# Kernel tuning notes

Measured on AMD Instinct MI355X. Metric: run time of the kernel, lower is better.

## Reference

```python
import jax, jax.numpy as jnp
import numpy as np

B, C, T = 2, 2, 4
N_SRC = 49152   # npix at level 6 (12 * 4^6)
N_TGT = 12288   # npix at level 5 (12 * 4^5)
D = 128


def setup_inputs() -> dict:
    key = jax.random.key(0)
    k1, k2, k3, k4 = jax.random.split(key, 4)
    x = jax.random.normal(k1, (B, C, T, N_SRC, D), dtype=jnp.float32)
    parent_map = jax.random.randint(k2, (N_SRC,), 0, N_TGT)
    W = jax.random.normal(k3, (D, D), dtype=jnp.float32) * 0.05  # Conv1d kernel_size=1 weight [out,in]
    b = jax.random.normal(k4, (D,), dtype=jnp.float32) * 0.05    # Conv1d bias
    return {"x": x, "parent_map": parent_map, "W": W, "b": b}


def reference(x, parent_map, W, b):
    # HEALPix downsample: scatter-add mean pooling over parent_map, then 1x1 conv.
    Bs, Cs, Ts, N, Dd = x.shape
    # flatten (b c t) and put pixel axis first for segment_sum: [N, BCT, D]
    x2 = x.reshape(Bs * Cs * Ts, N, Dd).transpose(1, 0, 2)
    sums = jax.ops.segment_sum(x2, parent_map, num_segments=N_TGT)          # [N_TGT, BCT, D]
    cnt = jax.ops.segment_sum(jnp.ones((N,), x.dtype), parent_map, num_segments=N_TGT)
    mean = sums / jnp.clip(cnt, 1e-6)[:, None, None]
    # 1x1 Conv1d over channel dim D: y = W @ mean + b
    out = jnp.einsum('mbd,ed->mbe', mean, W) + b                            # [N_TGT, BCT, D]
    return out.transpose(1, 0, 2).reshape(Bs, Cs, Ts, N_TGT, Dd)
```

## Files before the change

kernel.cpp:

```cpp
#include <hip/hip_runtime.h>
#include <stdint.h>

#define NSRC 49152
#define NTGT 12288
#define DIM  128
#define BCT  16
#define MPER 8
#define ROWS (MPER*BCT)
#define CAP  32

using short8  = __attribute__((ext_vector_type(8))) short;
using short4v = __attribute__((ext_vector_type(4))) short;
using bf16x8  = __attribute__((ext_vector_type(8))) __bf16;
using f32x4   = __attribute__((ext_vector_type(4))) float;

__device__ __forceinline__ short f2bf(float f){
  unsigned int u = __float_as_uint(f);
  return (short)((u + 0x7fffu + ((u >> 16) & 1u)) >> 16);
}

__global__ void k_scatter(const int* __restrict__ pm,
                          int* __restrict__ counts, int* __restrict__ child){
  int i = blockIdx.x * blockDim.x + threadIdx.x;
  if (i < NSRC){
    int p = pm[i];
    int pos = atomicAdd(&counts[p], 1);
    if (pos < CAP) child[p * CAP + pos] = i;
  }
}

__global__ void k_wprep(const float* __restrict__ W, short* __restrict__ Wt){
  int t  = blockIdx.x * blockDim.x + threadIdx.x;
  int e  = t & 127;
  int kk = t >> 7;
  const float4* src = (const float4*)(W + (size_t)e * DIM + kk * 8);
  float4 u = src[0], v = src[1];
  short8 h;
  h[0]=f2bf(u.x); h[1]=f2bf(u.y); h[2]=f2bf(u.z); h[3]=f2bf(u.w);
  h[4]=f2bf(v.x); h[5]=f2bf(v.y); h[6]=f2bf(v.z); h[7]=f2bf(v.w);
  *reinterpret_cast<short8*>(Wt + ((size_t)kk * 128 + e) * 8) = h;
}

__global__ __launch_bounds__(256, 4) void k_fused(
    const float* __restrict__ x, const short* __restrict__ Wt,
    const float* __restrict__ bias,
    const int* __restrict__ counts, const int* __restrict__ child,
    float* __restrict__ out)
{
  __shared__ __align__(16) short s_mean[ROWS * DIM];
  const int tid = threadIdx.x;
  const int m0  = blockIdx.x * MPER;

  {
    const int o = tid & 7;
    #pragma unroll
    for (int it = 0; it < 4; ++it){
      const int r   = it * 32 + (tid >> 3);
      const int m   = m0 + (r >> 4);
      const int bct = r & 15;
      int cnt = counts[m]; cnt = (cnt > CAP) ? CAP : cnt;
      const int* cl = child + (size_t)m * CAP;
      const float* rowb = x + (size_t)bct * NSRC * DIM;
      float4 acc[4];
      #pragma unroll
      for (int s = 0; s < 4; ++s) acc[s] = make_float4(0.f, 0.f, 0.f, 0.f);
      int c = 0;
      for (; c + 1 < cnt; c += 2){
        const int n0 = cl[c], n1 = cl[c + 1];
        const float4* p0 = (const float4*)(rowb + (size_t)n0 * DIM) + o;
        const float4* p1 = (const float4*)(rowb + (size_t)n1 * DIM) + o;
        float4 v0[4], v1[4];
        #pragma unroll
        for (int s = 0; s < 4; ++s) v0[s] = p0[s * 8];
        #pragma unroll
        for (int s = 0; s < 4; ++s) v1[s] = p1[s * 8];
        #pragma unroll
        for (int s = 0; s < 4; ++s){
          acc[s].x += v0[s].x + v1[s].x; acc[s].y += v0[s].y + v1[s].y;
          acc[s].z += v0[s].z + v1[s].z; acc[s].w += v0[s].w + v1[s].w;
        }
      }
      if (c < cnt){
        const int n0 = cl[c];
        const float4* p0 = (const float4*)(rowb + (size_t)n0 * DIM) + o;
        #pragma unroll
        for (int s = 0; s < 4; ++s){
          float4 v = p0[s * 8];
          acc[s].x += v.x; acc[s].y += v.y; acc[s].z += v.z; acc[s].w += v.w;
        }
      }
      const float inv = (cnt > 0) ? (1.0f / (float)cnt) : 0.0f;
      const int rsw = (r & 7) << 3;
      #pragma unroll
      for (int s = 0; s < 4; ++s){
        const int col = s * 32 + o * 4;
        short4v h;
        h[0] = f2bf(acc[s].x * inv); h[1] = f2bf(acc[s].y * inv);
        h[2] = f2bf(acc[s].z * inv); h[3] = f2bf(acc[s].w * inv);
        *reinterpret_cast<short4v*>(&s_mean[r * DIM + (col ^ rsw)]) = h;
      }
    }
  }

  __syncthreads();

  {
    const int w  = tid >> 6;
    const int l  = tid & 63;
    const int lr = l & 15;
    const int kg = l >> 4;
    f32x4 acc[2][8];
    #pragma unroll
    for (int i = 0; i < 2; ++i)
      #pragma unroll
      for (int n = 0; n < 8; ++n) acc[i][n] = (f32x4){0.f, 0.f, 0.f, 0.f};

    #pragma unroll 1
    for (int ks = 0; ks < 4; ++ks){
      const int k = ks * 32 + kg * 8;
      bf16x8 af[2];
      #pragma unroll
      for (int i = 0; i < 2; ++i){
        const int row = w * 32 + i * 16 + lr;
        af[i] = *reinterpret_cast<bf16x8*>(&s_mean[row * DIM + (k ^ ((row & 7) << 3))]);
      }
      const short* wp = Wt + ((size_t)(ks * 4 + kg) * 128 + lr) * 8;
      #pragma unroll
      for (int n = 0; n < 8; ++n){
        bf16x8 bfr = *reinterpret_cast<const bf16x8*>(wp + n * 128);
        acc[0][n] = __builtin_amdgcn_mfma_f32_16x16x32_bf16(af[0], bfr, acc[0][n], 0, 0, 0);
        acc[1][n] = __builtin_amdgcn_mfma_f32_16x16x32_bf16(af[1], bfr, acc[1][n], 0, 0, 0);
      }
    }

    float bv[8];
    #pragma unroll
    for (int n = 0; n < 8; ++n) bv[n] = bias[n * 16 + lr];

    #pragma unroll
    for (int i = 0; i < 2; ++i){
      #pragma unroll
      for (int j = 0; j < 4; ++j){
        const int gr  = w * 32 + i * 16 + (l >> 4) * 4 + j;
        const int m   = m0 + (gr >> 4);
        const int bct = gr & 15;
        float* po = out + ((size_t)bct * NTGT + m) * DIM;
        #pragma unroll
        for (int n = 0; n < 8; ++n) po[n * 16 + lr] = acc[i][n][j] + bv[n];
      }
    }
  }
}

extern "C" void kernel_launch(void* const* d_in, const int* in_sizes, int n_in,
                              void* d_out, int out_size, void* d_ws, size_t ws_size,
                              hipStream_t stream) {
  const float* x    = (const float*)d_in[0];
  const int*   pm   = (const int*)  d_in[1];
  const float* W    = (const float*)d_in[2];
  const float* bias = (const float*)d_in[3];
  float* out = (float*)d_out;

  int*   counts = (int*)d_ws;
  int*   child  = counts + NTGT;
  short* Wt     = (short*)(child + NTGT * CAP);

  hipMemsetAsync(counts, 0, NTGT * sizeof(int), stream);
  k_scatter<<<NSRC/256, 256, 0, stream>>>(pm, counts, child);
  k_wprep  <<<8, 256, 0, stream>>>(W, Wt);
  k_fused  <<<NTGT/MPER, 256, 0, stream>>>(x, Wt, bias, counts, child, out);
}
```

Baseline: 137.9 us.

## Stage output through LDS for coalesced nontemporal stores; merge setup kernels

The output epilogue now writes MFMA accumulators into a padded LDS tile in two rounds, then reads them back so each wavefront emits contiguous 16-byte nontemporal stores per bct row. This replaces the scattered 4-byte global stores of the old epilogue. Separately, the scatter and weight-prep kernels are merged into one launch to cut launch overhead. The change adds extra syncthreads and LDS traffic in the epilogue, and the LDS buffer grows from 32KB to about 33KB, which may affect occupancy.

```diff
diff --git a/kernel.cpp b/kernel.cpp
--- a/kernel.cpp
+++ b/kernel.cpp
@@ -4,10 +4,10 @@
 #define NSRC 49152
 #define NTGT 12288
 #define DIM  128
-#define BCT  16
 #define MPER 8
-#define ROWS (MPER*BCT)
+#define ROWS (MPER*16)
 #define CAP  32
+#define OSTR 132
 
 using short8  = __attribute__((ext_vector_type(8))) short;
 using short4v = __attribute__((ext_vector_type(4))) short;
@@ -19,26 +19,26 @@
   return (short)((u + 0x7fffu + ((u >> 16) & 1u)) >> 16);
 }
 
-__global__ void k_scatter(const int* __restrict__ pm,
-                          int* __restrict__ counts, int* __restrict__ child){
-  int i = blockIdx.x * blockDim.x + threadIdx.x;
-  if (i < NSRC){
+__global__ void k_setup(const int* __restrict__ pm,
+                        int* __restrict__ counts, int* __restrict__ child,
+                        const float* __restrict__ W, short* __restrict__ Wt){
+  const int b = blockIdx.x;
+  if (b < 192){
+    int i = b * 256 + threadIdx.x;
     int p = pm[i];
     int pos = atomicAdd(&counts[p], 1);
     if (pos < CAP) child[p * CAP + pos] = i;
+  } else {
+    int t  = (b - 192) * 256 + threadIdx.x;
+    int e  = t & 127;
+    int kk = t >> 7;
+    const float4* src = (const float4*)(W + (size_t)e * DIM + kk * 8);
+    float4 u = src[0], v = src[1];
+    short8 h;
+    h[0]=f2bf(u.x); h[1]=f2bf(u.y); h[2]=f2bf(u.z); h[3]=f2bf(u.w);
+    h[4]=f2bf(v.x); h[5]=f2bf(v.y); h[6]=f2bf(v.z); h[7]=f2bf(v.w);
+    *reinterpret_cast<short8*>(Wt + ((size_t)kk * 128 + e) * 8) = h;
   }
-}
-
-__global__ void k_wprep(const float* __restrict__ W, short* __restrict__ Wt){
-  int t  = blockIdx.x * blockDim.x + threadIdx.x;
-  int e  = t & 127;
-  int kk = t >> 7;
-  const float4* src = (const float4*)(W + (size_t)e * DIM + kk * 8);
-  float4 u = src[0], v = src[1];
-  short8 h;
-  h[0]=f2bf(u.x); h[1]=f2bf(u.y); h[2]=f2bf(u.z); h[3]=f2bf(u.w);
-  h[4]=f2bf(v.x); h[5]=f2bf(v.y); h[6]=f2bf(v.z); h[7]=f2bf(v.w);
-  *reinterpret_cast<short8*>(Wt + ((size_t)kk * 128 + e) * 8) = h;
 }
 
 __global__ __launch_bounds__(256, 4) void k_fused(
@@ -47,7 +47,9 @@
     const int* __restrict__ counts, const int* __restrict__ child,
     float* __restrict__ out)
 {
-  __shared__ __align__(16) short s_mean[ROWS * DIM];
+  __shared__ __align__(16) char smem[64 * OSTR * 4];
+  short* s_mean = (short*)smem;
+  float* s_out  = (float*)smem;
   const int tid = threadIdx.x;
   const int m0  = blockIdx.x * MPER;
 
@@ -104,49 +106,63 @@
 
   __syncthreads();
 
-  {
-    const int w  = tid >> 6;
-    const int l  = tid & 63;
-    const int lr = l & 15;
-    const int kg = l >> 4;
-    f32x4 acc[2][8];
+  const int w  = tid >> 6;
+  const int l  = tid & 63;
+  const int lr = l & 15;
+  const int kg = l >> 4;
+  f32x4 acc[2][8];
+  #pragma unroll
+  for (int i = 0; i < 2; ++i)
     #pragma unroll
-    for (int i = 0; i < 2; ++i)
-      #pragma unroll
-      for (int n = 0; n < 8; ++n) acc[i][n] = (f32x4){0.f, 0.f, 0.f, 0.f};
+    for (int n = 0; n < 8; ++n) acc[i][n] = (f32x4){0.f, 0.f, 0.f, 0.f};
 
-    #pragma unroll 1
-    for (int ks = 0; ks < 4; ++ks){
-      const int k = ks * 32 + kg * 8;
-      bf16x8 af[2];
-      #pragma unroll
-      for (int i = 0; i < 2; ++i){
-        const int row = w * 32 + i * 16 + lr;
-        af[i] = *reinterpret_cast<bf16x8*>(&s_mean[row * DIM + (k ^ ((row & 7) << 3))]);
-      }
-      const short* wp = Wt + ((size_t)(ks * 4 + kg) * 128 + lr) * 8;
-      #pragma unroll
-      for (int n = 0; n < 8; ++n){
-        bf16x8 bfr = *reinterpret_cast<const bf16x8*>(wp + n * 128);
-        acc[0][n] = __builtin_amdgcn_mfma_f32_16x16x32_bf16(af[0], bfr, acc[0][n], 0, 0, 0);
-        acc[1][n] = __builtin_amdgcn_mfma_f32_16x16x32_bf16(af[1], bfr, acc[1][n], 0, 0, 0);
-      }
-    }
-
-    float bv[8];
-    #pragma unroll
-    for (int n = 0; n < 8; ++n) bv[n] = bias[n * 16 + lr];
-
+  #pragma unroll 1
+  for (int ks = 0; ks < 4; ++ks){
+    const int k = ks * 32 + kg * 8;
+    bf16x8 af[2];
     #pragma unroll
     for (int i = 0; i < 2; ++i){
+      const int row = w * 32 + i * 16 + lr;
+      af[i] = *reinterpret_cast<bf16x8*>(&s_mean[row * DIM + (k ^ ((row & 7) << 3))]);
+    }
+    const short* wp = Wt + ((size_t)(ks * 4 + kg) * 128 + lr) * 8;
+    #pragma unroll
+    for (int n = 0; n < 8; ++n){
+      bf16x8 bfr = *reinterpret_cast<const bf16x8*>(wp + n * 128);
+      acc[0][n] = __builtin_amdgcn_mfma_f32_16x16x32_bf16(af[0], bfr, acc[0][n], 0, 0, 0);
+      acc[1][n] = __builtin_amdgcn_mfma_f32_16x16x32_bf16(af[1], bfr, acc[1][n], 0, 0, 0);
+    }
+  }
+
+  float bv[8];
+  #pragma unroll
+  for (int n = 0; n < 8; ++n) bv[n] = bias[n * 16 + lr];
+
+  #pragma unroll
+  for (int round = 0; round < 2; ++round){
+    __syncthreads();
+    if ((w >> 1) == round){
       #pragma unroll
-      for (int j = 0; j < 4; ++j){
-        const int gr  = w * 32 + i * 16 + (l >> 4) * 4 + j;
-        const int m   = m0 + (gr >> 4);
-        const int bct = gr & 15;
-        float* po = out + ((size_t)bct * NTGT + m) * DIM;
+      for (int i = 0; i < 2; ++i)
         #pragma unroll
-        for (int n = 0; n < 8; ++n) po[n * 16 + lr] = acc[i][n][j] + bv[n];
+        for (int j = 0; j < 4; ++j){
+          const int grl = (w & 1) * 32 + i * 16 + (l >> 4) * 4 + j;
+          #pragma unroll
+          for (int n = 0; n < 8; ++n)
+            s_out[grl * OSTR + n * 16 + lr] = acc[i][n][j] + bv[n];
+        }
+    }
+    __syncthreads();
+    #pragma unroll
+    for (int r2 = 0; r2 < 4; ++r2){
+      const int bct = w * 4 + r2;
+      #pragma unroll
+      for (int it2 = 0; it2 < 2; ++it2){
+        const int f  = it2 * 64 + l;
+        const int mi = f >> 5, d4 = f & 31;
+        f32x4 v = *reinterpret_cast<f32x4*>(&s_out[(mi * 16 + bct) * OSTR + d4 * 4]);
+        float* gp = out + ((size_t)bct * NTGT + m0 + round * 4 + mi) * DIM + d4 * 4;
+        __builtin_nontemporal_store(v, reinterpret_cast<f32x4*>(gp));
       }
     }
   }
@@ -166,7 +182,6 @@
   short* Wt     = (short*)(child + NTGT * CAP);
 
   hipMemsetAsync(counts, 0, NTGT * sizeof(int), stream);
-  k_scatter<<<NSRC/256, 256, 0, stream>>>(pm, counts, child);
-  k_wprep  <<<8, 256, 0, stream>>>(W, Wt);
-  k_fused  <<<NTGT/MPER, 256, 0, stream>>>(x, Wt, bias, counts, child, out);
+  k_setup<<<200, 256, 0, stream>>>(pm, counts, child, W, Wt);
+  k_fused<<<NTGT/MPER, 256, 0, stream>>>(x, Wt, bias, counts, child, out);
 }
```

Result: faster. 123.9 us (-10.1%).
